# Optimization experiments

Hardware: AMD Instinct MI355X
Metric: run time of the kernel (lower is better)

## Reference

```python
import jax, jax.numpy as jnp
import numpy as np

B, S, DIM = 2, 2048, 2048
NH = 16
D_NOPE, D_ROPE, D_V = 128, 64, 128
D_QK = D_NOPE + D_ROPE  # 192
KV_RANK = 512
RMS_EPS = 1e-6


def setup_inputs() -> dict:
    key = jax.random.key(0)
    ks = jax.random.split(key, 8)
    x = jax.random.normal(ks[0], (B, S, DIM), dtype=jnp.float32)
    # rotary freqs as (cos, sin) pairs: [S, D_ROPE//2, 2]
    pos = jnp.arange(S, dtype=jnp.float32)
    inv_freq = 1.0 / (10000.0 ** (jnp.arange(0, D_ROPE, 2, dtype=jnp.float32) / D_ROPE))
    ang = pos[:, None] * inv_freq[None, :]
    freqs_cis = jnp.stack([jnp.cos(ang), jnp.sin(ang)], axis=-1)
    # causal mask [S, S]
    mask = jnp.where(jnp.arange(S)[None, :] > jnp.arange(S)[:, None], -jnp.inf, 0.0).astype(jnp.float32)
    sd = lambda k, shp, fan: jax.random.normal(k, shp, dtype=jnp.float32) * (fan ** -0.5)
    wq = sd(ks[1], (NH * D_QK, DIM), DIM)
    wkv_a = sd(ks[2], (KV_RANK + D_ROPE, DIM), DIM)
    wkv_b = sd(ks[3], (NH * (D_NOPE + D_V), KV_RANK), KV_RANK)
    wo = sd(ks[4], (DIM, NH * D_V), NH * D_V)
    kv_norm_w = jnp.ones((KV_RANK,), dtype=jnp.float32)
    return {"x": x, "start_pos": 0, "freqs_cis": freqs_cis, "mask": mask,
            "wq": wq, "wkv_a": wkv_a, "wkv_b": wkv_b, "wo": wo, "kv_norm_w": kv_norm_w}


def _rope(x, freqs):
    # x: [b, s, h, d] with d even; freqs: [s, d//2, 2] (cos, sin)
    b, s, h, d = x.shape
    xr = x.reshape(b, s, h, d // 2, 2)
    cos = freqs[None, :, None, :, 0]
    sin = freqs[None, :, None, :, 1]
    ye = xr[..., 0] * cos - xr[..., 1] * sin
    yo = xr[..., 0] * sin + xr[..., 1] * cos
    return jnp.stack([ye, yo], axis=-1).reshape(b, s, h, d)


def _rms_norm(x, w):
    var = jnp.mean(jnp.square(x), axis=-1, keepdims=True)
    return x * jax.lax.rsqrt(var + RMS_EPS) * w


def reference(x, start_pos, freqs_cis, mask, wq, wkv_a, wkv_b, wo, kv_norm_w):
    b, s, _ = x.shape
    scale = D_QK ** -0.5
    # query projection -> [b, s, h, d_qk]
    q = jnp.einsum('bsd,ed->bse', x, wq).reshape(b, s, NH, D_QK)
    q_nope, q_pe = q[..., :D_NOPE], q[..., D_NOPE:]
    q_pe = _rope(q_pe, freqs_cis)
    q = jnp.concatenate([q_nope, q_pe], axis=-1)
    # latent kv projection -> [b, s, kv_rank + d_rope]
    kv = jnp.einsum('bsd,ed->bse', x, wkv_a)
    kv_lat, k_pe = kv[..., :KV_RANK], kv[..., KV_RANK:]
    k_pe = _rope(k_pe[:, :, None, :], freqs_cis)  # [b, s, 1, d_rope]
    kv_up = jnp.einsum('bsr,er->bse', _rms_norm(kv_lat, kv_norm_w), wkv_b)
    kv_up = kv_up.reshape(b, s, NH, D_NOPE + D_V)
    k_nope, v = kv_up[..., :D_NOPE], kv_up[..., D_NOPE:]
    k = jnp.concatenate([k_nope, jnp.broadcast_to(k_pe, (b, s, NH, D_ROPE))], axis=-1)
    # start_pos = 0 prefill: cache[:end_pos] == freshly computed k, v
    scores = jnp.einsum('bshd,bthd->bsht', q, k) * scale
    if mask is not None:
        scores = scores + mask[None, :, None, :]
    probs = jax.nn.softmax(scores.astype(jnp.float32), axis=-1).astype(x.dtype)
    out = jnp.einsum('bsht,bthd->bshd', probs, v)
    return jnp.einsum('bse,de->bsd', out.reshape(b, s, NH * D_V), wo)
```

## Files before the change

kernel.cpp:

```cpp
#include <hip/hip_runtime.h>
#include <hip/hip_bf16.h>


typedef __bf16 bf16x8 __attribute__((ext_vector_type(8)));
typedef float  f32x4  __attribute__((ext_vector_type(4)));
typedef float  f32x16 __attribute__((ext_vector_type(16)));
typedef unsigned short us8 __attribute__((ext_vector_type(8)));
typedef unsigned short us4 __attribute__((ext_vector_type(4)));
typedef unsigned int   ui4 __attribute__((ext_vector_type(4)));

#define S_LEN   2048
#define BS_TOT  4096
#define NH      16
#define DQK     192
#define DV      128
#define KV_RANK 512
#define QSTR    3840

__device__ inline unsigned short f2bf(float f) {
  __hip_bfloat16 h = __float2bfloat16(f);
  return *reinterpret_cast<unsigned short*>(&h);
}
__device__ inline float bfu2f(unsigned short u) {
  unsigned int x = ((unsigned int)u) << 16;
  return __builtin_bit_cast(float, x);
}
__device__ inline unsigned int pack2bf(float a, float b) {
  return (unsigned int)f2bf(a) | ((unsigned int)f2bf(b) << 16);
}
__device__ inline void glds16(const void* g, void* l) {
  __builtin_amdgcn_global_load_lds(
      (const __attribute__((address_space(1))) unsigned int*)g,
      (__attribute__((address_space(3))) unsigned int*)l, 16, 0, 0);
}

__global__ __launch_bounds__(256) void cast_all_kernel(
    const float* __restrict__ x, const float* __restrict__ wq,
    const float* __restrict__ wkva, const float* __restrict__ wkvb,
    const float* __restrict__ wo,
    __hip_bfloat16* __restrict__ xb, __hip_bfloat16* __restrict__ wqb,
    __hip_bfloat16* __restrict__ wkvab, __hip_bfloat16* __restrict__ wkvbb,
    __hip_bfloat16* __restrict__ wob) {
  const int bid = blockIdx.x;
  const float* src; __hip_bfloat16* dst; int n, npad, b0, nb;
  if (bid < 771)       { src = x;    dst = xb;    n = 8388608; npad = 8388608; b0 = 0;    nb = 771; }
  else if (bid < 1349) { src = wq;   dst = wqb;   n = 6291456; npad = 6291456; b0 = 771;  nb = 578; }
  else if (bid < 1469) { src = wkva; dst = wkvab; n = 1179648; npad = 1572864; b0 = 1349; nb = 120; }
  else if (bid < 1662) { src = wkvb; dst = wkvbb; n = 2097152; npad = 2097152; b0 = 1469; nb = 193; }
  else                 { src = wo;   dst = wob;   n = 4194304; npad = 4194304; b0 = 1662; nb = 386; }
  const int tid = (bid - b0) * 256 + threadIdx.x;
  const int stride = nb * 256;
  for (int i = tid * 4; i < npad; i += stride * 4) {
    if (i + 3 < n) {
      f32x4 v = *(const f32x4*)(src + i);
      dst[i + 0] = __float2bfloat16(v.x);
      dst[i + 1] = __float2bfloat16(v.y);
      dst[i + 2] = __float2bfloat16(v.z);
      dst[i + 3] = __float2bfloat16(v.w);
    } else {
#pragma unroll
      for (int z = 0; z < 4; z++)
        dst[i + z] = __float2bfloat16((i + z < n) ? src[i + z] : 0.f);
    }
  }
}

template<int OUT_BF16>
__global__ __launch_bounds__(512, 1) void gemm_bt256(
    const __hip_bfloat16* __restrict__ A, const __hip_bfloat16* __restrict__ Bw,
    void* __restrict__ Cp, int M, int N, int K, int nbx) {
  __shared__ alignas(16) unsigned short Ah[2][2][128 * 64];
  __shared__ alignas(16) unsigned short Bh[2][2][128 * 64];

  const int nwg = gridDim.x;
  const int cpx = nwg >> 3;
  const int id  = (blockIdx.x & 7) * cpx + (blockIdx.x >> 3);
  const int bx = id % nbx, by = id / nbx;
  const int m0 = by * 256, n0 = bx * 256;

  const int tid = threadIdx.x, w = tid >> 6, lane = tid & 63;
  const int wr = w >> 2, wc = w & 3;
  const int ml = lane & 15, quad = lane >> 4;
  const int srow = w * 8 + (lane >> 3);
  const int scol = ((lane & 7) ^ (lane >> 3)) * 8;

  const unsigned short* Ag = (const unsigned short*)A + (size_t)(m0 + srow) * K + scol;
  const unsigned short* Bg = (const unsigned short*)Bw + (size_t)(n0 + srow) * K + scol;

  f32x4 acc[2][2][4][2];
#pragma unroll
  for (int a = 0; a < 2; a++)
#pragma unroll
    for (int bq = 0; bq < 2; bq++)
#pragma unroll
      for (int i = 0; i < 4; i++)
#pragma unroll
        for (int j = 0; j < 2; j++)
#pragma unroll
          for (int e = 0; e < 4; e++) acc[a][bq][i][j][e] = 0.0f;

  auto stageA = [&](int ha, int par, int k0) {
#pragma unroll
    for (int j = 0; j < 2; j++)
      glds16(Ag + (size_t)(ha * 128 + j * 64) * K + k0,
             &Ah[ha][par][(j * 64 + w * 8) * 64]);
  };
  auto stageB = [&](int hb, int par, int k0) {
#pragma unroll
    for (int j = 0; j < 2; j++)
      glds16(Bg + (size_t)(hb * 128 + j * 64) * K + k0,
             &Bh[hb][par][(j * 64 + w * 8) * 64]);
  };

  const int nt = K / 64;
  stageA(0, 0, 0); stageB(0, 0, 0); stageA(1, 0, 0); stageB(1, 0, 0);
  if (nt > 1) { stageA(0, 1, 64); stageB(0, 1, 64); }
  asm volatile("s_waitcnt vmcnt(4)" ::: "memory");
  __builtin_amdgcn_s_barrier();
  asm volatile("" ::: "memory");

  for (int u = 0; u < nt; ++u) {
    const int P = u & 1;
#pragma unroll
    for (int q = 0; q < 4; ++q) {
      const int ha = q >> 1, hb = q & 1;
      const unsigned short* As = &Ah[ha][P][0];
      const unsigned short* Bs = &Bh[hb][P][0];

      bf16x8 af[4][2], bf[2][2];
#pragma unroll
      for (int mf = 0; mf < 4; mf++) {
        int r = wr * 64 + mf * 16 + ml;
        const char* rowp = (const char*)&As[r * 64];
#pragma unroll
        for (int ks = 0; ks < 2; ks++)
          af[mf][ks] =
              *(const bf16x8*)(rowp + ((ks * 64 + quad * 16) ^ ((ml & 7) << 4)));
      }
#pragma unroll
      for (int nf = 0; nf < 2; nf++) {
        int r = wc * 32 + nf * 16 + ml;
        const char* rowp = (const char*)&Bs[r * 64];
#pragma unroll
        for (int ks = 0; ks < 2; ks++)
          bf[nf][ks] =
              *(const bf16x8*)(rowp + ((ks * 64 + quad * 16) ^ ((ml & 7) << 4)));
      }

      if (q == 0) { if (u + 1 < nt) stageA(1, (u + 1) & 1, (u + 1) * 64); }
      if (q == 1) { if (u + 1 < nt) stageB(1, (u + 1) & 1, (u + 1) * 64); }
      if (q == 2) { if (u + 2 < nt) stageA(0, P, (u + 2) * 64); }
      if (q == 3) {
        if (u + 2 < nt) stageB(0, P, (u + 2) * 64);
        asm volatile("s_waitcnt vmcnt(4)" ::: "memory");
      }

      asm volatile("" ::: "memory");
      __builtin_amdgcn_s_barrier();
      asm volatile("s_waitcnt lgkmcnt(0)" ::: "memory");
      __builtin_amdgcn_sched_barrier(0);

      __builtin_amdgcn_s_setprio(1);
#pragma unroll
      for (int mf = 0; mf < 4; mf++)
#pragma unroll
        for (int nf = 0; nf < 2; nf++)
#pragma unroll
          for (int ks = 0; ks < 2; ks++)
            acc[ha][hb][mf][nf] = __builtin_amdgcn_mfma_f32_16x16x32_bf16(
                af[mf][ks], bf[nf][ks], acc[ha][hb][mf][nf], 0, 0, 0);
      __builtin_amdgcn_s_setprio(0);

      asm volatile("" ::: "memory");
      __builtin_amdgcn_s_barrier();
      asm volatile("" ::: "memory");
    }
  }

#pragma unroll
  for (int ha = 0; ha < 2; ha++) {
#pragma unroll
    for (int hb = 0; hb < 2; hb++) {
#pragma unroll
      for (int mf = 0; mf < 4; mf++) {
#pragma unroll
        for (int nf = 0; nf < 2; nf++) {
          int col = n0 + hb * 128 + wc * 32 + nf * 16 + ml;
          int rowb = m0 + ha * 128 + wr * 64 + mf * 16 + quad * 4;
#pragma unroll
          for (int j = 0; j < 4; j++) {
            float v = acc[ha][hb][mf][nf][j];
            if (OUT_BF16)
              ((__hip_bfloat16*)Cp)[(size_t)(rowb + j) * N + col] = __float2bfloat16(v);
            else
              ((float*)Cp)[(size_t)(rowb + j) * N + col] = v;
          }
        }
      }
    }
  }
}

__global__ __launch_bounds__(256) void rope_rms_kernel(
    __hip_bfloat16* __restrict__ qkv, const float* __restrict__ w,
    const float* __restrict__ freqs, __hip_bfloat16* __restrict__ latent,
    __hip_bfloat16* __restrict__ kpe_out) {
  int si = blockIdx.x;
  int s  = si & (S_LEN - 1);
  int tid = threadIdx.x;
#pragma unroll
  for (int p = tid; p < NH * 32; p += 256) {
    int h = p >> 5, i = p & 31;
    size_t base = (size_t)si * QSTR + h * DQK + 128 + 2 * i;
    float c  = freqs[s * 64 + 2 * i];
    float sn = freqs[s * 64 + 2 * i + 1];
    float x0 = __bfloat162float(qkv[base]);
    float x1 = __bfloat162float(qkv[base + 1]);
    qkv[base]     = __float2bfloat16(x0 * c - x1 * sn);
    qkv[base + 1] = __float2bfloat16(x0 * sn + x1 * c);
  }
  const unsigned short* row = (const unsigned short*)qkv + (size_t)si * QSTR + 3072;
  float v0 = bfu2f(row[tid]), v1 = bfu2f(row[tid + 256]);
  float ss = v0 * v0 + v1 * v1;
#pragma unroll
  for (int off = 1; off < 64; off <<= 1) ss += __shfl_xor(ss, off, 64);
  __shared__ float red[4];
  if ((tid & 63) == 0) red[tid >> 6] = ss;
  __syncthreads();
  float tot = red[0] + red[1] + red[2] + red[3];
  float r = rsqrtf(tot / 512.0f + 1e-6f);
  latent[(size_t)si * 512 + tid]       = __float2bfloat16(v0 * r * w[tid]);
  latent[(size_t)si * 512 + tid + 256] = __float2bfloat16(v1 * r * w[tid + 256]);
  if (tid < 32) {
    float c  = freqs[s * 64 + 2 * tid];
    float sn = freqs[s * 64 + 2 * tid + 1];
    float x0 = bfu2f(row[512 + 2 * tid]), x1 = bfu2f(row[512 + 2 * tid + 1]);
    kpe_out[(size_t)si * 64 + 2 * tid]     = __float2bfloat16(x0 * c - x1 * sn);
    kpe_out[(size_t)si * 64 + 2 * tid + 1] = __float2bfloat16(x0 * sn + x1 * c);
  }
}

__global__ __launch_bounds__(512, 2) void attn_mfma_kernel(
    const __hip_bfloat16* __restrict__ qb,
    const __hip_bfloat16* __restrict__ kvup,
    const __hip_bfloat16* __restrict__ kpe,
    unsigned short* __restrict__ op0,
    unsigned short* __restrict__ op1,
    float* __restrict__ mlp0,
    float* __restrict__ mlp1) {
  constexpr int KS = 200;
  constexpr int VS = 36;
  __shared__ alignas(16) unsigned short Ks[2][64 * KS];
  __shared__ alignas(16) unsigned int   Vt2[2][128 * VS];

  const int id = blockIdx.x;
  const int x  = id >> 5;
  const int hb = id & 31;
  const int h  = hb >> 1, b = hb & 1;

  const int tid = threadIdx.x, wave = tid >> 6, lane = tid & 63;
  const int l31 = lane & 31, hh = lane >> 5;
  const float qs2 = 0.07216878364870322f * 1.4426950408889634f;

  const int m16 = tid & 15;
  const int hp  = tid >> 4;
  const int vkey = (m16 & 7) << 2;
  const unsigned short* kvbase = (const unsigned short*)kvup;
  const unsigned short* kpbase = (const unsigned short*)kpe;

  int kr_[3], kc_[3];
#pragma unroll
  for (int it = 0; it < 3; it++) {
    int slot = tid + it * 512;
    kr_[it] = slot / 24;
    kc_[it] = slot - kr_[it] * 24;
  }

#pragma unroll 1
  for (int item = 0; item < 2; ++item) {
    const int qt2    = item ? (7 - x) : x;
    const int kstart = item ? (2 * qt2 + 2) : 0;
    const int kend   = kstart + 2 * qt2 + 2;
    const int qwb = qt2 * 256 + wave * 32;
    const int qg  = qwb + l31;

    bf16x8 Qf[12];
    {
      const unsigned short* qrow = (const unsigned short*)qb +
          (size_t)(b * S_LEN + qg) * QSTR + h * DQK;
#pragma unroll
      for (int s = 0; s < 12; s++)
        Qf[s] = *(const bf16x8*)(qrow + s * 16 + hh * 8);
    }

    float m_i = -1e30f, l_i = 0.0f;
    f32x16 O2[4];
#pragma unroll
    for (int mt = 0; mt < 4; mt++)
#pragma unroll
      for (int j = 0; j < 16; j++) O2[mt][j] = 0.0f;

    us8 Kpre[3], Vpre[2];

    const unsigned short* kptr[3];
    int kstep[3];
#pragma unroll
    for (int it = 0; it < 3; it++) {
      if (kc_[it] < 16) {
        kptr[it] = kvbase + (size_t)(b * S_LEN + kstart * 64 + kr_[it]) * (NH * 256)
                   + h * 256 + kc_[it] * 8;
        kstep[it] = 64 * NH * 256;
      } else {
        kptr[it] = kpbase + (size_t)(b * S_LEN + kstart * 64 + kr_[it]) * 64
                   + (kc_[it] - 16) * 8;
        kstep[it] = 64 * 64;
      }
    }
    const unsigned short* vptr = kvbase +
        (size_t)(b * S_LEN + kstart * 64 + 2 * hp) * (NH * 256) + h * 256 + 128 + m16 * 8;

    if (item) __syncthreads();

    {
#pragma unroll
      for (int it = 0; it < 3; it++) {
        Kpre[it] = *(const us8*)kptr[it];
        kptr[it] += kstep[it];
      }
      Vpre[0] = *(const us8*)vptr;
      Vpre[1] = *(const us8*)(vptr + NH * 256);
      vptr += 64 * NH * 256;
#pragma unroll
      for (int it = 0; it < 3; it++)
        *(us8*)&Ks[0][kr_[it] * KS + kc_[it] * 8] = Kpre[it];
#pragma unroll
      for (int z = 0; z < 8; z++) {
        int d = m16 * 8 + z;
        Vt2[0][d * VS + (hp ^ vkey)] =
            (unsigned)(unsigned short)Vpre[0][z] |
            ((unsigned)(unsigned short)Vpre[1][z] << 16);
      }
      __syncthreads();
    }

    int cur = 0;
    for (int kt = kstart; kt < kend; kt++) {
      const int kb = kt * 64;
      const unsigned short* ksc = Ks[cur];
      const unsigned int*   vtc = Vt2[cur];

      const int havenext = (kt + 1 < kend);
      if (havenext) {
#pragma unroll
        for (int it = 0; it < 3; it++) {
          Kpre[it] = *(const us8*)kptr[it];
          kptr[it] += kstep[it];
        }
        Vpre[0] = *(const us8*)vptr;
        Vpre[1] = *(const us8*)(vptr + NH * 256);
        vptr += 64 * NH * 256;
      }

      if (kb <= qwb + 31) {
        f32x16 st2[2];
        __builtin_amdgcn_s_setprio(1);
#pragma unroll
        for (int mt = 0; mt < 2; mt++) {
          f32x16 acc;
#pragma unroll
          for (int j = 0; j < 16; j++) acc[j] = 0.0f;
#pragma unroll
          for (int s = 0; s < 12; s++) {
            bf16x8 kf = *(const bf16x8*)&ksc[(mt * 32 + l31) * KS + s * 16 + hh * 8];
            acc = __builtin_amdgcn_mfma_f32_32x32x16_bf16(kf, Qf[s], acc, 0, 0, 0);
          }
          st2[mt] = acc;
        }
        __builtin_amdgcn_s_setprio(0);

        if (kb + 64 > qwb) {
#pragma unroll
          for (int mt = 0; mt < 2; mt++)
#pragma unroll
            for (int r = 0; r < 16; r++) {
              int kpos = kb + mt * 32 + (r & 3) + 8 * (r >> 2) + 4 * hh;
              st2[mt][r] = (kpos > qg) ? -1e30f : st2[mt][r];
            }
        }
        float t16[16];
#pragma unroll
        for (int r = 0; r < 16; r++) t16[r] = fmaxf(st2[0][r], st2[1][r]);
#pragma unroll
        for (int sw = 8; sw >= 1; sw >>= 1)
#pragma unroll
          for (int r = 0; r < 8; r++)
            if (r < sw) t16[r] = fmaxf(t16[r], t16[r + sw]);
        float mloc = t16[0] * qs2;
        mloc = fmaxf(mloc, __shfl_xor(mloc, 32, 64));
        if (!__all(mloc <= m_i + 8.0f)) {
          float m_new = fmaxf(m_i, mloc);
          float alpha = exp2f(m_i - m_new);
          l_i *= alpha;
#pragma unroll
          for (int mt = 0; mt < 4; mt++)
#pragma unroll
            for (int j = 0; j < 16; j++) O2[mt][j] *= alpha;
          m_i = m_new;
        }
        const float nm = -m_i;
#pragma unroll
        for (int mt = 0; mt < 2; mt++)
#pragma unroll
          for (int r = 0; r < 16; r++) {
            float p = exp2f(fmaf(st2[mt][r], qs2, nm));
            st2[mt][r] = p;
          }
        float s16[16];
#pragma unroll
        for (int r = 0; r < 16; r++) s16[r] = st2[0][r] + st2[1][r];
#pragma unroll
        for (int sw = 8; sw >= 1; sw >>= 1)
#pragma unroll
          for (int r = 0; r < 8; r++)
            if (r < sw) s16[r] += s16[r + sw];
        float psum = s16[0];
        psum += __shfl_xor(psum, 32, 64);
        l_i += psum;

        bf16x8 pf[4];
#pragma unroll
        for (int ss = 0; ss < 4; ss++) {
          const int pmt = ss >> 1, gg = ss & 1;
          unsigned int U0 = pack2bf(st2[pmt][gg * 8 + 0], st2[pmt][gg * 8 + 1]);
          unsigned int U1 = pack2bf(st2[pmt][gg * 8 + 2], st2[pmt][gg * 8 + 3]);
          unsigned int U2 = pack2bf(st2[pmt][gg * 8 + 4], st2[pmt][gg * 8 + 5]);
          unsigned int U3 = pack2bf(st2[pmt][gg * 8 + 6], st2[pmt][gg * 8 + 7]);
          unsigned int E0 = __shfl_xor(hh ? U0 : U2, 32, 64);
          unsigned int E1 = __shfl_xor(hh ? U1 : U3, 32, 64);
          ui4 pd;
          pd.x = hh ? E0 : U0;
          pd.y = hh ? E1 : U1;
          pd.z = hh ? U2 : E0;
          pd.w = hh ? U3 : E1;
          pf[ss] = __builtin_bit_cast(bf16x8, pd);
        }

        __builtin_amdgcn_s_setprio(1);
#pragma unroll
        for (int ss = 0; ss < 4; ss++) {
#pragma unroll
          for (int mt = 0; mt < 4; mt++) {
            int v = mt * 32 + l31;
            const unsigned int* vp =
                &vtc[v * VS + ((ss * 8 + hh * 4) ^ (((v >> 3) & 7) << 2))];
            bf16x8 bv = *(const bf16x8*)vp;
            O2[mt] = __builtin_amdgcn_mfma_f32_32x32x16_bf16(bv, pf[ss], O2[mt],
                                                             0, 0, 0);
          }
        }
        __builtin_amdgcn_s_setprio(0);
      }

      if (havenext) {
#pragma unroll
        for (int it = 0; it < 3; it++)
          *(us8*)&Ks[cur ^ 1][kr_[it] * KS + kc_[it] * 8] = Kpre[it];
#pragma unroll
        for (int z = 0; z < 8; z++) {
          int d = m16 * 8 + z;
          Vt2[cur ^ 1][d * VS + (hp ^ vkey)] =
              (unsigned)(unsigned short)Vpre[0][z] |
              ((unsigned)(unsigned short)Vpre[1][z] << 16);
        }
        __syncthreads();
        cur ^= 1;
      }
    }

    unsigned short* op = item ? op1 : op0;
    float* mlp = item ? mlp1 : mlp0;
    const size_t basep = (size_t)(b * S_LEN + qg) * NH + h;
    unsigned short* orow = op + basep * 128;
#pragma unroll
    for (int mt = 0; mt < 4; mt++) {
#pragma unroll
      for (int g = 0; g < 4; g++) {
        us4 pk;
#pragma unroll
        for (int j = 0; j < 4; j++) pk[j] = f2bf(O2[mt][g * 4 + j]);
        *(us4*)(orow + mt * 32 + g * 8 + hh * 4) = pk;
      }
    }
    if (hh == 0) {
      mlp[basep * 2 + 0] = m_i;
      mlp[basep * 2 + 1] = l_i;
    }
  }
}

__global__ __launch_bounds__(256) void attn_combine_kernel(
    const unsigned short* __restrict__ op0, const unsigned short* __restrict__ op1,
    const float* __restrict__ mlp0, const float* __restrict__ mlp1,
    __hip_bfloat16* __restrict__ attn_out) {
  const int bs = blockIdx.x;
  const int tid = threadIdx.x;
  const int h = tid >> 4, dc = (tid & 15) * 8;
  const size_t basep = (size_t)bs * NH + h;
  const us8 a = *(const us8*)(op0 + basep * 128 + dc);
  const us8 c = *(const us8*)(op1 + basep * 128 + dc);
  const float m0 = mlp0[basep * 2], l0 = mlp0[basep * 2 + 1];
  const float m1 = mlp1[basep * 2], l1 = mlp1[basep * 2 + 1];
  const float m = fmaxf(m0, m1);
  const float a0 = exp2f(m0 - m), a1 = exp2f(m1 - m);
  const float inv = 1.0f / (l0 * a0 + l1 * a1);
  us8 o;
#pragma unroll
  for (int z = 0; z < 8; z++) {
    float v = (bfu2f((unsigned short)a[z]) * a0 +
               bfu2f((unsigned short)c[z]) * a1) * inv;
    o[z] = f2bf(v);
  }
  *(us8*)((unsigned short*)attn_out + (size_t)bs * (NH * DV) + h * DV + dc) = o;
}

extern "C" void kernel_launch(void* const* d_in, const int* in_sizes, int n_in,
                              void* d_out, int out_size, void* d_ws, size_t ws_size,
                              hipStream_t stream) {
  const float* x     = (const float*)d_in[0];
  const float* freqs = (const float*)d_in[2];
  const float* wq    = (const float*)d_in[4];
  const float* wkva  = (const float*)d_in[5];
  const float* wkvb  = (const float*)d_in[6];
  const float* wo    = (const float*)d_in[7];
  const float* kvnw  = (const float*)d_in[8];
  float* out = (float*)d_out;

  char* ws = (char*)d_ws;
  size_t off = 0;
  auto alloc = [&](size_t bytes) {
    void* p = ws + off;
    off += (bytes + 255) & ~(size_t)255;
    return p;
  };
  __hip_bfloat16* x_bf    = (__hip_bfloat16*)alloc((size_t)BS_TOT * 2048 * 2);
  __hip_bfloat16* wq_bf   = (__hip_bfloat16*)alloc((size_t)3072 * 2048 * 2);
  __hip_bfloat16* wkva_bf = (__hip_bfloat16*)alloc((size_t)768 * 2048 * 2);
  __hip_bfloat16* wkvb_bf = (__hip_bfloat16*)alloc((size_t)4096 * 512 * 2);
  __hip_bfloat16* wo_bf   = (__hip_bfloat16*)alloc((size_t)2048 * 2048 * 2);
  __hip_bfloat16* qkv_bf  = (__hip_bfloat16*)alloc((size_t)BS_TOT * QSTR * 2);
  __hip_bfloat16* latent  = (__hip_bfloat16*)alloc((size_t)BS_TOT * 512 * 2);
  __hip_bfloat16* kpe     = (__hip_bfloat16*)alloc((size_t)BS_TOT * 64 * 2);
  __hip_bfloat16* kvup    = (__hip_bfloat16*)alloc((size_t)BS_TOT * 4096 * 2);
  __hip_bfloat16* attn    = (__hip_bfloat16*)alloc((size_t)BS_TOT * 2048 * 2);

  unsigned short* op0 = (unsigned short*)x_bf;
  unsigned short* op1 = (unsigned short*)wq_bf;
  float* mlp0 = (float*)latent;
  float* mlp1 = mlp0 + (size_t)BS_TOT * NH * 2;

  cast_all_kernel<<<2048, 256, 0, stream>>>(x, wq, wkva, wkvb, wo,
                                            x_bf, wq_bf, wkva_bf, wkvb_bf, wo_bf);

  gemm_bt256<1><<<dim3(240), 512, 0, stream>>>(
      x_bf, wq_bf, qkv_bf, BS_TOT, QSTR, 2048, QSTR / 256);
  rope_rms_kernel<<<BS_TOT, 256, 0, stream>>>(qkv_bf, kvnw, freqs, latent, kpe);

  gemm_bt256<1><<<dim3(256), 512, 0, stream>>>(
      latent, wkvb_bf, kvup, BS_TOT, 4096, 512, 16);

  attn_mfma_kernel<<<dim3(256, 1, 1), 512, 0, stream>>>(
      qkv_bf, kvup, kpe, op0, op1, mlp0, mlp1);
  attn_combine_kernel<<<dim3(BS_TOT, 1, 1), 256, 0, stream>>>(
      op0, op1, mlp0, mlp1, attn);

  gemm_bt256<0><<<dim3(128), 512, 0, stream>>>(
      attn, wo_bf, out, BS_TOT, 2048, 2048, 8);
}
```

Baseline: 268.9 us.

## Reuse LDS fragments across quadrants in GEMM main loop and drop per-quadrant syncs

The GEMM main loop now reads the A fragments once per half and both B fragment sets once per k-tile, reusing them across the four quadrant MFMA blocks instead of re-reading A and B from LDS for every quadrant. It also removes the per-quadrant lgkmcnt wait and the barrier between fragment reads and MFMAs, cutting one barrier per quadrant and interleaving the global-to-LDS staging differently. The aim is to lower LDS read traffic and synchronisation overhead. In exchange it raises register pressure (extra B fragments), and it relies on the implicit wait ordering staying correct with the new stage placement.

```diff
diff --git a/kernel.cpp b/kernel.cpp
--- a/kernel.cpp
+++ b/kernel.cpp
@@ -112,6 +112,29 @@
              &Bh[hb][par][(j * 64 + w * 8) * 64]);
   };
 
+  auto readA = [&](bf16x8 (&af)[4][2], const unsigned short* As) {
+#pragma unroll
+    for (int mf = 0; mf < 4; mf++) {
+      int r = wr * 64 + mf * 16 + ml;
+      const char* rowp = (const char*)&As[r * 64];
+#pragma unroll
+      for (int ks = 0; ks < 2; ks++)
+        af[mf][ks] =
+            *(const bf16x8*)(rowp + ((ks * 64 + quad * 16) ^ ((ml & 7) << 4)));
+    }
+  };
+  auto readB = [&](bf16x8 (&bf)[2][2], const unsigned short* Bs) {
+#pragma unroll
+    for (int nf = 0; nf < 2; nf++) {
+      int r = wc * 32 + nf * 16 + ml;
+      const char* rowp = (const char*)&Bs[r * 64];
+#pragma unroll
+      for (int ks = 0; ks < 2; ks++)
+        bf[nf][ks] =
+            *(const bf16x8*)(rowp + ((ks * 64 + quad * 16) ^ ((ml & 7) << 4)));
+    }
+  };
+
   const int nt = K / 64;
   stageA(0, 0, 0); stageB(0, 0, 0); stageA(1, 0, 0); stageB(1, 0, 0);
   if (nt > 1) { stageA(0, 1, 64); stageB(0, 1, 64); }
@@ -121,60 +144,76 @@
 
   for (int u = 0; u < nt; ++u) {
     const int P = u & 1;
-#pragma unroll
-    for (int q = 0; q < 4; ++q) {
-      const int ha = q >> 1, hb = q & 1;
-      const unsigned short* As = &Ah[ha][P][0];
-      const unsigned short* Bs = &Bh[hb][P][0];
-
-      bf16x8 af[4][2], bf[2][2];
-#pragma unroll
-      for (int mf = 0; mf < 4; mf++) {
-        int r = wr * 64 + mf * 16 + ml;
-        const char* rowp = (const char*)&As[r * 64];
+    bf16x8 af[4][2], b0f[2][2], b1f[2][2];
+
+    if (u + 1 < nt) stageA(1, (u + 1) & 1, (u + 1) * 64);
+    readA(af, &Ah[0][P][0]);
+    readB(b0f, &Bh[0][P][0]);
+    readB(b1f, &Bh[1][P][0]);
+    __builtin_amdgcn_s_setprio(1);
+#pragma unroll
+    for (int mf = 0; mf < 4; mf++)
+#pragma unroll
+      for (int nf = 0; nf < 2; nf++)
 #pragma unroll
         for (int ks = 0; ks < 2; ks++)
-          af[mf][ks] =
-              *(const bf16x8*)(rowp + ((ks * 64 + quad * 16) ^ ((ml & 7) << 4)));
-      }
-#pragma unroll
-      for (int nf = 0; nf < 2; nf++) {
-        int r = wc * 32 + nf * 16 + ml;
-        const char* rowp = (const char*)&Bs[r * 64];
+          acc[0][0][mf][nf] = __builtin_amdgcn_mfma_f32_16x16x32_bf16(
+              af[mf][ks], b0f[nf][ks], acc[0][0][mf][nf], 0, 0, 0);
+    __builtin_amdgcn_s_setprio(0);
+    asm volatile("" ::: "memory");
+    __builtin_amdgcn_s_barrier();
+    asm volatile("" ::: "memory");
+
+    if (u + 1 < nt) stageB(1, (u + 1) & 1, (u + 1) * 64);
+    __builtin_amdgcn_s_setprio(1);
+#pragma unroll
+    for (int mf = 0; mf < 4; mf++)
+#pragma unroll
+      for (int nf = 0; nf < 2; nf++)
 #pragma unroll
         for (int ks = 0; ks < 2; ks++)
-          bf[nf][ks] =
-              *(const bf16x8*)(rowp + ((ks * 64 + quad * 16) ^ ((ml & 7) << 4)));
-      }
-
-      if (q == 0) { if (u + 1 < nt) stageA(1, (u + 1) & 1, (u + 1) * 64); }
-      if (q == 1) { if (u + 1 < nt) stageB(1, (u + 1) & 1, (u + 1) * 64); }
-      if (q == 2) { if (u + 2 < nt) stageA(0, P, (u + 2) * 64); }
-      if (q == 3) {
-        if (u + 2 < nt) stageB(0, P, (u + 2) * 64);
-        asm volatile("s_waitcnt vmcnt(4)" ::: "memory");
-      }
-
-      asm volatile("" ::: "memory");
-      __builtin_amdgcn_s_barrier();
-      asm volatile("s_waitcnt lgkmcnt(0)" ::: "memory");
-      __builtin_amdgcn_sched_barrier(0);
-
-      __builtin_amdgcn_s_setprio(1);
-#pragma unroll
-      for (int mf = 0; mf < 4; mf++)
-#pragma unroll
-        for (int nf = 0; nf < 2; nf++)
-#pragma unroll
-          for (int ks = 0; ks < 2; ks++)
-            acc[ha][hb][mf][nf] = __builtin_amdgcn_mfma_f32_16x16x32_bf16(
-                af[mf][ks], bf[nf][ks], acc[ha][hb][mf][nf], 0, 0, 0);
-      __builtin_amdgcn_s_setprio(0);
-
-      asm volatile("" ::: "memory");
-      __builtin_amdgcn_s_barrier();
-      asm volatile("" ::: "memory");
-    }
+          acc[0][1][mf][nf] = __builtin_amdgcn_mfma_f32_16x16x32_bf16(
+              af[mf][ks], b1f[nf][ks], acc[0][1][mf][nf], 0, 0, 0);
+    __builtin_amdgcn_s_setprio(0);
+    asm volatile("" ::: "memory");
+    __builtin_amdgcn_s_barrier();
+    asm volatile("" ::: "memory");
+
+    if (u + 2 < nt) stageA(0, P, (u + 2) * 64);
+    readA(af, &Ah[1][P][0]);
+    __builtin_amdgcn_s_setprio(1);
+#pragma unroll
+    for (int mf = 0; mf < 4; mf++)
+#pragma unroll
+      for (int nf = 0; nf < 2; nf++)
+#pragma unroll
+        for (int ks = 0; ks < 2; ks++)
+          acc[1][0][mf][nf] = __builtin_amdgcn_mfma_f32_16x16x32_bf16(
+              af[mf][ks], b0f[nf][ks], acc[1][0][mf][nf], 0, 0, 0);
+    __builtin_amdgcn_s_setprio(0);
+    asm volatile("" ::: "memory");
+    __builtin_amdgcn_s_barrier();
+    asm volatile("" ::: "memory");
+
+    if (u + 2 < nt) {
+      stageB(0, P, (u + 2) * 64);
+      asm volatile("s_waitcnt vmcnt(4)" ::: "memory");
+    } else {
+      asm volatile("s_waitcnt vmcnt(0)" ::: "memory");
+    }
+    __builtin_amdgcn_s_setprio(1);
+#pragma unroll
+    for (int mf = 0; mf < 4; mf++)
+#pragma unroll
+      for (int nf = 0; nf < 2; nf++)
+#pragma unroll
+        for (int ks = 0; ks < 2; ks++)
+          acc[1][1][mf][nf] = __builtin_amdgcn_mfma_f32_16x16x32_bf16(
+              af[mf][ks], b1f[nf][ks], acc[1][1][mf][nf], 0, 0, 0);
+    __builtin_amdgcn_s_setprio(0);
+    asm volatile("" ::: "memory");
+    __builtin_amdgcn_s_barrier();
+    asm volatile("" ::: "memory");
   }
 
 #pragma unroll
```

Measured after the change: 268.2 us. No clear change (-0.3%).
